# Kernel tuning notes

Hardware: AMD Instinct MI355X
Metric: run time of the kernel (lower is better)

The kernel has to match this reference:

```python
import jax, jax.numpy as jnp
from jax import lax
import numpy as np

B, T, F_IN, H = 64, 128, 12, 128  # batch, seq_len, input/output features, hidden


def _uinit(key, shape, fan):
    return jax.random.uniform(key, shape, jnp.float32, -1.0, 1.0) / np.float32(np.sqrt(fan))


def setup_inputs() -> dict:
    key = jax.random.key(0)
    ks = jax.random.split(key, 12)
    inp = {
        "x": jax.random.normal(ks[0], (B, T, F_IN), jnp.float32),
        # encoder LSTM (gate order i,f,g,o; b = b_ih + b_hh folded together)
        "enc_Wih": _uinit(ks[1], (4 * H, F_IN), H),
        "enc_Whh": _uinit(ks[2], (4 * H, H), H),
        "enc_b": _uinit(ks[3], (4 * H,), H),
        # decoder LSTM (input is the 12-dim teacher-forced x slice)
        "dec_Wih": _uinit(ks[4], (4 * H, F_IN), H),
        "dec_Whh": _uinit(ks[5], (4 * H, H), H),
        "dec_b": _uinit(ks[6], (4 * H,), H),
        # attention: Linear(2H -> H) with bias, then v: Linear(H -> 1, no bias)
        "attn_W": _uinit(ks[7], (H, 2 * H), 2 * H),
        "attn_b": _uinit(ks[8], (H,), 2 * H),
        "v_w": _uinit(ks[9], (H,), H),
        # output layer: Linear(2H -> F_IN)  (intended width; see notes)
        "out_W": _uinit(ks[10], (F_IN, 2 * H), 2 * H),
        "out_b": _uinit(ks[11], (F_IN,), 2 * H),
    }
    return inp


def _lstm_cell(xt, h, c, Wih, Whh, b):
    z = xt @ Wih.T + h @ Whh.T + b  # [B, 4H]
    i, f, g, o = jnp.split(z, 4, axis=-1)
    c = jax.nn.sigmoid(f) * c + jax.nn.sigmoid(i) * jnp.tanh(g)
    h = jax.nn.sigmoid(o) * jnp.tanh(c)
    return h, c


def reference(x, enc_Wih, enc_Whh, enc_b, dec_Wih, dec_Whh, dec_b,
              attn_W, attn_b, v_w, out_W, out_b):
    b_, t_, _ = x.shape
    hdim = enc_Whh.shape[1]
    xs = jnp.swapaxes(x, 0, 1)  # [T, B, F]
    h0 = jnp.zeros((b_, hdim), x.dtype)
    c0 = jnp.zeros((b_, hdim), x.dtype)

    def enc_step(carry, xt):
        h, c = carry
        h, c = _lstm_cell(xt, h, c, enc_Wih, enc_Whh, enc_b)
        return (h, c), h

    (hT, cT), enc_hs = lax.scan(enc_step, (h0, c0), xs)
    enc_out = jnp.swapaxes(enc_hs, 0, 1)  # [B, T, H]

    # split attn weight: cat(hidden, enc_out) @ W.T == hidden@W1.T + enc_out@W2.T
    W1, W2 = attn_W[:, :hdim], attn_W[:, hdim:]
    enc_proj = jnp.einsum("bth,gh->btg", enc_out, W2)  # precompute encoder side

    def dec_step(carry, xt):
        h, c = carry
        h, c = _lstm_cell(xt, h, c, dec_Wih, dec_Whh, dec_b)
        energy = jnp.tanh((h @ W1.T)[:, None, :] + enc_proj + attn_b)  # [B,T,H]
        score = jnp.einsum("bth,h->bt", energy, v_w)
        w = jax.nn.softmax(score, axis=1)  # attention over encoder time
        ctx = jnp.einsum("bt,bth->bh", w, enc_out)
        return (h, c), jnp.concatenate([h, ctx], axis=-1)  # [B, 2H]

    _, dec_ys = lax.scan(dec_step, (hT, cT), xs)
    dec_out = jnp.swapaxes(dec_ys, 0, 1)  # [B, T, 2H]
    return dec_out @ out_W.T + out_b  # [B, T, F]
```

## Files before the change

### kernel.cpp

```cpp
#include <hip/hip_runtime.h>
#include <hip/hip_bf16.h>

#define BB 64
#define TT 128
#define FIN 12
#define HH 128
#define GG 512

#define LOG2E 1.4426950408889634f
#define TWO_LOG2E 2.8853900817779268f

__device__ __forceinline__ float fexp2(float x) { return __builtin_amdgcn_exp2f(x); }
__device__ __forceinline__ float frcp(float x)  { return __builtin_amdgcn_rcpf(x); }

__device__ __forceinline__ float tanh_f(float x) {
  return 1.0f - 2.0f * frcp(1.0f + fexp2(TWO_LOG2E * x));
}
__device__ __forceinline__ float sigm_f(float x) {
  return frcp(1.0f + fexp2(-LOG2E * x));
}

#define FMA4S(acc, s, v) do { \
  acc.x = fmaf((s), (v).x, acc.x); \
  acc.y = fmaf((s), (v).y, acc.y); \
  acc.z = fmaf((s), (v).z, acc.z); \
  acc.w = fmaf((s), (v).w, acc.w); } while (0)

__global__ __launch_bounds__(512, 2) void lstm_kernel(
    const float* __restrict__ x,
    const float* __restrict__ eWih, const float* __restrict__ eWhh, const float* __restrict__ eb,
    const float* __restrict__ dWih, const float* __restrict__ dWhh, const float* __restrict__ db,
    float* __restrict__ encH, float* __restrict__ decH)
{
  const int b = blockIdx.x;
  const int g = threadIdx.x;

  __shared__ __align__(16) float xs[TT * FIN];
  __shared__ __align__(16) float h_lds[HH];
  __shared__ __align__(16) float zact[GG];

  if (g < (TT * FIN / 4))
    ((float4*)xs)[g] = ((const float4*)(x + (size_t)b * TT * FIN))[g];
  if (g < HH) h_lds[g] = 0.0f;
  float c = 0.0f;

  const int gate = g >> 7;

  #pragma unroll 1
  for (int phase = 0; phase < 2; ++phase) {
    const float* Wih  = phase ? dWih : eWih;
    const float* Whh  = phase ? dWhh : eWhh;
    const float* bias = phase ? db : eb;
    float* Hout       = phase ? decH : encH;

    float wih[FIN];
    #pragma unroll
    for (int j = 0; j < 3; ++j) {
      float4 v = *(const float4*)(Wih + g * FIN + 4 * j);
      wih[4*j+0] = v.x; wih[4*j+1] = v.y; wih[4*j+2] = v.z; wih[4*j+3] = v.w;
    }
    float whh[HH];
    #pragma unroll
    for (int j = 0; j < 32; ++j) {
      float4 v = *(const float4*)(Whh + g * HH + 4 * j);
      whh[4*j+0] = v.x; whh[4*j+1] = v.y; whh[4*j+2] = v.z; whh[4*j+3] = v.w;
    }
    const float bz = bias[g];

    #pragma unroll 1
    for (int t = 0; t < TT; ++t) {
      __syncthreads();
      float a0 = bz, a1 = 0.0f, a2 = 0.0f, a3 = 0.0f;
      {
        const float4* xt4 = (const float4*)(xs + t * FIN);
        float4 xa = xt4[0], xb = xt4[1], xc = xt4[2];
        a0 = fmaf(xa.x, wih[0], a0); a1 = fmaf(xa.y, wih[1], a1);
        a2 = fmaf(xa.z, wih[2], a2); a3 = fmaf(xa.w, wih[3], a3);
        a0 = fmaf(xb.x, wih[4], a0); a1 = fmaf(xb.y, wih[5], a1);
        a2 = fmaf(xb.z, wih[6], a2); a3 = fmaf(xb.w, wih[7], a3);
        a0 = fmaf(xc.x, wih[8], a0); a1 = fmaf(xc.y, wih[9], a1);
        a2 = fmaf(xc.z, wih[10], a2); a3 = fmaf(xc.w, wih[11], a3);
      }
      #pragma unroll
      for (int k = 0; k < HH; k += 4) {
        float4 h4 = *(const float4*)&h_lds[k];
        a0 = fmaf(h4.x, whh[k + 0], a0);
        a1 = fmaf(h4.y, whh[k + 1], a1);
        a2 = fmaf(h4.z, whh[k + 2], a2);
        a3 = fmaf(h4.w, whh[k + 3], a3);
      }
      float acc = (a0 + a1) + (a2 + a3);
      zact[g] = (gate == 2) ? tanh_f(acc) : sigm_f(acc);
      __syncthreads();
      if (g < HH) {
        float iv = zact[g], fv = zact[HH + g], gv = zact[2 * HH + g], ov = zact[3 * HH + g];
        c = fmaf(fv, c, iv * gv);
        float hn = ov * tanh_f(c);
        h_lds[g] = hn;
        Hout[((size_t)b * TT + t) * HH + g] = hn;
      }
    }
  }
}

__global__ __launch_bounds__(256, 2) void proj_kernel(
    const float* __restrict__ encH, const float* __restrict__ decH,
    const float* __restrict__ attnW, const float* __restrict__ attnb,
    float* __restrict__ Abuf, float* __restrict__ Pbuf)
{
  const int m  = blockIdx.x & 1;
  const int b  = (blockIdx.x >> 1) & 63;
  const int r0 = (blockIdx.x >> 7) * 16;
  const int tid = threadIdx.x;

  __shared__ __align__(16) float WT[64 * 128];
  __shared__ __align__(16) float Xt[16 * 128];

  const float* X = (m ? encH : decH) + ((size_t)b * TT + r0) * HH;
  const float* W = attnW + (m ? HH : 0);

  ((float4*)Xt)[tid]       = ((const float4*)X)[tid];
  ((float4*)Xt)[256 + tid] = ((const float4*)X)[256 + tid];

  const int hq = tid & 31, rr = tid >> 5;
  const int h0 = 4 * hq;

  float4 acc0, acc1;
  if (m == 0) { acc0 = *(const float4*)(attnb + h0); acc1 = acc0; }
  else        { acc0 = make_float4(0.f, 0.f, 0.f, 0.f); acc1 = acc0; }

  for (int kb = 0; kb < 2; ++kb) {
    __syncthreads();
    {
      int h = tid >> 1, koff = (tid & 1) * 32;
      #pragma unroll
      for (int j = 0; j < 8; ++j) {
        float4 v = *(const float4*)(W + h * 256 + kb * 64 + koff + 4 * j);
        int kp = koff + 4 * j;
        WT[(kp + 0) * 128 + h] = v.x;
        WT[(kp + 1) * 128 + h] = v.y;
        WT[(kp + 2) * 128 + h] = v.z;
        WT[(kp + 3) * 128 + h] = v.w;
      }
    }
    __syncthreads();
    const float* xr0 = Xt + (2 * rr) * 128 + kb * 64;
    const float* xr1 = xr0 + 128;
    #pragma unroll
    for (int k4 = 0; k4 < 64; k4 += 4) {
      float4 xa = *(const float4*)(xr0 + k4);
      float4 xb = *(const float4*)(xr1 + k4);
      float4 w0 = *(const float4*)&WT[(k4 + 0) * 128 + h0];
      float4 w1 = *(const float4*)&WT[(k4 + 1) * 128 + h0];
      float4 w2 = *(const float4*)&WT[(k4 + 2) * 128 + h0];
      float4 w3 = *(const float4*)&WT[(k4 + 3) * 128 + h0];
      FMA4S(acc0, xa.x, w0); FMA4S(acc0, xa.y, w1);
      FMA4S(acc0, xa.z, w2); FMA4S(acc0, xa.w, w3);
      FMA4S(acc1, xb.x, w0); FMA4S(acc1, xb.y, w1);
      FMA4S(acc1, xb.z, w2); FMA4S(acc1, xb.w, w3);
    }
  }
  float* O = (m ? Pbuf : Abuf) + ((size_t)b * TT + r0) * HH;
  *(float4*)(O + (2 * rr) * 128 + h0)     = acc0;
  *(float4*)(O + (2 * rr + 1) * 128 + h0) = acc1;
}

__global__ __launch_bounds__(512, 2) void attn_kernel(
    const float* __restrict__ encH, const float* __restrict__ decH,
    const float* __restrict__ Abuf, const float* __restrict__ Pbuf,
    const float* __restrict__ vw, const float* __restrict__ outW,
    const float* __restrict__ outb, float* __restrict__ out)
{
  const int b  = blockIdx.x >> 3;
  const int s0 = (blockIdx.x & 7) * 16;
  const int tid = threadIdx.x;

  __shared__ __align__(16) float buf[64 * 128];
  __shared__ __align__(16) float a_lds[16 * 128];
  __shared__ __align__(16) float sc[16 * 128];
  __shared__ __align__(16) float dh[16 * 128];
  __shared__ __align__(16) float vl[HH];

  ((float4*)a_lds)[tid] = ((const float4*)(Abuf + ((size_t)b * TT + s0) * HH))[tid];
  ((float4*)dh)[tid]    = ((const float4*)(decH + ((size_t)b * TT + s0) * HH))[tid];
  if (tid < 32) ((float4*)vl)[tid] = ((const float4*)vw)[tid];

  const int u  = tid & 31;
  const int sl = tid >> 5;
  const int uq = u & 15;
  const int uh = u >> 4;

  for (int half = 0; half < 2; ++half) {
    const int tbase = half * 64;
    __syncthreads();
    #pragma unroll
    for (int i = 0; i < 4; ++i) {
      int flat = i * 2048 + tid * 4;
      int tp = flat >> 7;
      int h0 = flat & 127;
      float4 v = *(const float4*)(Pbuf + ((size_t)b * TT + tbase + tp) * HH + h0);
      int tq = tp >> 2, tr = tp & 3;
      buf[(h0 + 0) * 64 + 4 * ((tq ^ ((h0 + 0) >> 2)) & 15) + tr] = v.x;
      buf[(h0 + 1) * 64 + 4 * ((tq ^ ((h0 + 1) >> 2)) & 15) + tr] = v.y;
      buf[(h0 + 2) * 64 + 4 * ((tq ^ ((h0 + 2) >> 2)) & 15) + tr] = v.z;
      buf[(h0 + 3) * 64 + 4 * ((tq ^ ((h0 + 3) >> 2)) & 15) + tr] = v.w;
    }
    __syncthreads();
    float4 acc = make_float4(0.f, 0.f, 0.f, 0.f);
    const float* arow = a_lds + sl * 128;
    #pragma unroll 8
    for (int hh = 0; hh < 64; ++hh) {
      int h = uh * 64 + hh;
      float ah = arow[h];
      float vh = vl[h];
      float4 p4 = *(const float4*)&buf[h * 64 + 4 * ((uq ^ ((h >> 2) & 15)) & 15)];
      acc.x = fmaf(vh, tanh_f(ah + p4.x), acc.x);
      acc.y = fmaf(vh, tanh_f(ah + p4.y), acc.y);
      acc.z = fmaf(vh, tanh_f(ah + p4.z), acc.z);
      acc.w = fmaf(vh, tanh_f(ah + p4.w), acc.w);
    }
    acc.x += __shfl_xor(acc.x, 16, 64);
    acc.y += __shfl_xor(acc.y, 16, 64);
    acc.z += __shfl_xor(acc.z, 16, 64);
    acc.w += __shfl_xor(acc.w, 16, 64);
    if (uh == 0) *(float4*)&sc[sl * 128 + tbase + 4 * uq] = acc;
  }
  __syncthreads();

  {
    float4 sv = *(const float4*)&sc[sl * 128 + 4 * u];
    float mx = fmaxf(fmaxf(sv.x, sv.y), fmaxf(sv.z, sv.w));
    #pragma unroll
    for (int msk = 1; msk <= 16; msk <<= 1) mx = fmaxf(mx, __shfl_xor(mx, msk, 64));
    float4 e;
    e.x = fexp2(LOG2E * (sv.x - mx));
    e.y = fexp2(LOG2E * (sv.y - mx));
    e.z = fexp2(LOG2E * (sv.z - mx));
    e.w = fexp2(LOG2E * (sv.w - mx));
    float sm = (e.x + e.y) + (e.z + e.w);
    #pragma unroll
    for (int msk = 1; msk <= 16; msk <<= 1) sm += __shfl_xor(sm, msk, 64);
    float r = frcp(sm);
    e.x *= r; e.y *= r; e.z *= r; e.w *= r;
    *(float4*)&sc[sl * 128 + 4 * u] = e;
  }

  float4 ctx = make_float4(0.f, 0.f, 0.f, 0.f);
  const int h0c = 4 * u;
  for (int half = 0; half < 2; ++half) {
    const int tbase = half * 64;
    __syncthreads();
    #pragma unroll
    for (int i = 0; i < 4; ++i) {
      int flat = i * 2048 + tid * 4;
      int tp = flat >> 7;
      int hh0 = flat & 127;
      *(float4*)&buf[tp * 128 + hh0] =
          *(const float4*)(encH + ((size_t)b * TT + tbase + tp) * HH + hh0);
    }
    __syncthreads();
    const float* wrow = sc + sl * 128 + tbase;
    #pragma unroll 8
    for (int tp = 0; tp < 64; ++tp) {
      float wt = wrow[tp];
      float4 e4 = *(const float4*)&buf[tp * 128 + h0c];
      FMA4S(ctx, wt, e4);
    }
  }
  __syncthreads();
  *(float4*)&a_lds[sl * 128 + h0c] = ctx;
  __syncthreads();

  if (tid < 192) {
    int s = tid / 12, f = tid % 12;
    float acc = outb[f];
    const float4* w4 = (const float4*)(outW + f * 256);
    const float4* d4 = (const float4*)(dh + s * 128);
    const float4* c4 = (const float4*)(a_lds + s * 128);
    #pragma unroll
    for (int k = 0; k < 32; ++k) {
      float4 wv = w4[k], dv = d4[k];
      acc = fmaf(wv.x, dv.x, acc); acc = fmaf(wv.y, dv.y, acc);
      acc = fmaf(wv.z, dv.z, acc); acc = fmaf(wv.w, dv.w, acc);
    }
    #pragma unroll
    for (int k = 0; k < 32; ++k) {
      float4 wv = w4[32 + k], cv = c4[k];
      acc = fmaf(wv.x, cv.x, acc); acc = fmaf(wv.y, cv.y, acc);
      acc = fmaf(wv.z, cv.z, acc); acc = fmaf(wv.w, cv.w, acc);
    }
    out[((size_t)b * TT + s0 + s) * FIN + f] = acc;
  }
}

extern "C" void kernel_launch(void* const* d_in, const int* in_sizes, int n_in,
                              void* d_out, int out_size, void* d_ws, size_t ws_size,
                              hipStream_t stream)
{
  const float* x     = (const float*)d_in[0];
  const float* eWih  = (const float*)d_in[1];
  const float* eWhh  = (const float*)d_in[2];
  const float* eb    = (const float*)d_in[3];
  const float* dWih  = (const float*)d_in[4];
  const float* dWhh  = (const float*)d_in[5];
  const float* db    = (const float*)d_in[6];
  const float* attnW = (const float*)d_in[7];
  const float* attnb = (const float*)d_in[8];
  const float* vw    = (const float*)d_in[9];
  const float* outW  = (const float*)d_in[10];
  const float* outb  = (const float*)d_in[11];
  float* out = (float*)d_out;

  float* ws   = (float*)d_ws;
  const size_t SEG = (size_t)BB * TT * HH;
  float* encH = ws;
  float* decH = ws + SEG;
  float* Abuf = ws + 2 * SEG;
  float* Pbuf = ws + 3 * SEG;

  lstm_kernel<<<64, 512, 0, stream>>>(x, eWih, eWhh, eb, dWih, dWhh, db, encH, decH);
  proj_kernel<<<1024, 256, 0, stream>>>(encH, decH, attnW, attnb, Abuf, Pbuf);
  attn_kernel<<<512, 512, 0, stream>>>(encH, decH, Abuf, Pbuf, vw, outW, outb, out);
}
```

Baseline: 364.6 us.

## Split LSTM gate dot products across two thread halves with LDS reduction

The LSTM recurrence kernel now launches 1024 threads per batch row instead of 512, and each gate row's 128-wide hidden dot product (plus the 12-wide input part) is split into two halves handled by separate threads. Partial sums go to shared memory, and the 128 cell threads combine them, add bias and apply the activations. This halves the serial FMA chain and the per-thread weight registers on the latency-bound sequential path. In exchange it adds an LDS partial-sum exchange, moves all gate activations onto 128 threads, and runs larger blocks that need more barrier participants.

```diff
diff --git a/kernel.cpp b/kernel.cpp
--- a/kernel.cpp
+++ b/kernel.cpp
@@ -26,25 +26,25 @@
   acc.z = fmaf((s), (v).z, acc.z); \
   acc.w = fmaf((s), (v).w, acc.w); } while (0)
 
-__global__ __launch_bounds__(512, 2) void lstm_kernel(
+__global__ __launch_bounds__(1024, 4) void lstm_kernel(
     const float* __restrict__ x,
     const float* __restrict__ eWih, const float* __restrict__ eWhh, const float* __restrict__ eb,
     const float* __restrict__ dWih, const float* __restrict__ dWhh, const float* __restrict__ db,
     float* __restrict__ encH, float* __restrict__ decH)
 {
-  const int b = blockIdx.x;
-  const int g = threadIdx.x;
+  const int b   = blockIdx.x;
+  const int tid = threadIdx.x;
+  const int g   = tid & 511;
+  const int kh  = tid >> 9;
 
   __shared__ __align__(16) float xs[TT * FIN];
   __shared__ __align__(16) float h_lds[HH];
-  __shared__ __align__(16) float zact[GG];
-
-  if (g < (TT * FIN / 4))
-    ((float4*)xs)[g] = ((const float4*)(x + (size_t)b * TT * FIN))[g];
-  if (g < HH) h_lds[g] = 0.0f;
+  __shared__ __align__(16) float part[2 * GG];
+
+  if (tid < (TT * FIN / 4))
+    ((float4*)xs)[tid] = ((const float4*)(x + (size_t)b * TT * FIN))[tid];
+  if (tid < HH) h_lds[tid] = 0.0f;
   float c = 0.0f;
-
-  const int gate = g >> 7;
 
   #pragma unroll 1
   for (int phase = 0; phase < 2; ++phase) {
@@ -53,51 +53,58 @@
     const float* bias = phase ? db : eb;
     float* Hout       = phase ? decH : encH;
 
-    float wih[FIN];
-    #pragma unroll
-    for (int j = 0; j < 3; ++j) {
-      float4 v = *(const float4*)(Wih + g * FIN + 4 * j);
-      wih[4*j+0] = v.x; wih[4*j+1] = v.y; wih[4*j+2] = v.z; wih[4*j+3] = v.w;
-    }
-    float whh[HH];
-    #pragma unroll
-    for (int j = 0; j < 32; ++j) {
-      float4 v = *(const float4*)(Whh + g * HH + 4 * j);
-      whh[4*j+0] = v.x; whh[4*j+1] = v.y; whh[4*j+2] = v.z; whh[4*j+3] = v.w;
-    }
-    const float bz = bias[g];
+    float4 whh[16];
+    #pragma unroll
+    for (int j = 0; j < 16; ++j)
+      whh[j] = *(const float4*)(Whh + g * HH + kh * 64 + 4 * j);
+    float wih[6];
+    #pragma unroll
+    for (int j = 0; j < 6; ++j)
+      wih[j] = Wih[g * FIN + kh * 6 + j];
+
+    float b_i = 0.f, b_f = 0.f, b_g = 0.f, b_o = 0.f;
+    if (tid < HH) {
+      b_i = bias[tid];
+      b_f = bias[HH + tid];
+      b_g = bias[2 * HH + tid];
+      b_o = bias[3 * HH + tid];
+    }
 
     #pragma unroll 1
     for (int t = 0; t < TT; ++t) {
       __syncthreads();
-      float a0 = bz, a1 = 0.0f, a2 = 0.0f, a3 = 0.0f;
+      float a0, a1, a2 = 0.0f, a3 = 0.0f;
       {
-        const float4* xt4 = (const float4*)(xs + t * FIN);
-        float4 xa = xt4[0], xb = xt4[1], xc = xt4[2];
-        a0 = fmaf(xa.x, wih[0], a0); a1 = fmaf(xa.y, wih[1], a1);
-        a2 = fmaf(xa.z, wih[2], a2); a3 = fmaf(xa.w, wih[3], a3);
-        a0 = fmaf(xb.x, wih[4], a0); a1 = fmaf(xb.y, wih[5], a1);
-        a2 = fmaf(xb.z, wih[6], a2); a3 = fmaf(xb.w, wih[7], a3);
-        a0 = fmaf(xc.x, wih[8], a0); a1 = fmaf(xc.y, wih[9], a1);
-        a2 = fmaf(xc.z, wih[10], a2); a3 = fmaf(xc.w, wih[11], a3);
+        const float2* xt2 = (const float2*)(xs + t * FIN + kh * 6);
+        float2 x0 = xt2[0], x1 = xt2[1], x2 = xt2[2];
+        a0 = x0.x * wih[0]; a1 = x0.y * wih[1];
+        a0 = fmaf(x1.x, wih[2], a0); a1 = fmaf(x1.y, wih[3], a1);
+        a0 = fmaf(x2.x, wih[4], a0); a1 = fmaf(x2.y, wih[5], a1);
       }
+      const float* hbase = h_lds + kh * 64;
       #pragma unroll
-      for (int k = 0; k < HH; k += 4) {
-        float4 h4 = *(const float4*)&h_lds[k];
-        a0 = fmaf(h4.x, whh[k + 0], a0);
-        a1 = fmaf(h4.y, whh[k + 1], a1);
-        a2 = fmaf(h4.z, whh[k + 2], a2);
-        a3 = fmaf(h4.w, whh[k + 3], a3);
+      for (int k = 0; k < 64; k += 4) {
+        float4 h4 = *(const float4*)(hbase + k);
+        a0 = fmaf(h4.x, whh[k >> 2].x, a0);
+        a1 = fmaf(h4.y, whh[k >> 2].y, a1);
+        a2 = fmaf(h4.z, whh[k >> 2].z, a2);
+        a3 = fmaf(h4.w, whh[k >> 2].w, a3);
       }
-      float acc = (a0 + a1) + (a2 + a3);
-      zact[g] = (gate == 2) ? tanh_f(acc) : sigm_f(acc);
+      part[2 * g + kh] = (a0 + a1) + (a2 + a3);
       __syncthreads();
-      if (g < HH) {
-        float iv = zact[g], fv = zact[HH + g], gv = zact[2 * HH + g], ov = zact[3 * HH + g];
-        c = fmaf(fv, c, iv * gv);
-        float hn = ov * tanh_f(c);
-        h_lds[g] = hn;
-        Hout[((size_t)b * TT + t) * HH + g] = hn;
+      if (tid < HH) {
+        float2 pi = *(const float2*)&part[2 * tid];
+        float2 pf = *(const float2*)&part[2 * (HH + tid)];
+        float2 pg = *(const float2*)&part[2 * (2 * HH + tid)];
+        float2 po = *(const float2*)&part[2 * (3 * HH + tid)];
+        float zi = sigm_f(pi.x + pi.y + b_i);
+        float zf = sigm_f(pf.x + pf.y + b_f);
+        float zg = tanh_f(pg.x + pg.y + b_g);
+        float zo = sigm_f(po.x + po.y + b_o);
+        c = fmaf(zf, c, zi * zg);
+        float hn = zo * tanh_f(c);
+        h_lds[tid] = hn;
+        Hout[((size_t)b * TT + t) * HH + tid] = hn;
       }
     }
   }
@@ -318,7 +325,7 @@
   float* Abuf = ws + 2 * SEG;
   float* Pbuf = ws + 3 * SEG;
 
-  lstm_kernel<<<64, 512, 0, stream>>>(x, eWih, eWhh, eb, dWih, dWhh, db, encH, decH);
+  lstm_kernel<<<64, 1024, 0, stream>>>(x, eWih, eWhh, eb, dWih, dWhh, db, encH, decH);
   proj_kernel<<<1024, 256, 0, stream>>>(encH, decH, attnW, attnb, Abuf, Pbuf);
   attn_kernel<<<512, 512, 0, stream>>>(encH, decH, Abuf, Pbuf, vw, outW, outb, out);
 }
```

New measurement: 391.0 us. 1.07x slower.

## Pair LSTM gates per lane with shuffle exchange, one barrier per step

Applied to the files above, without the earlier changes.

The LSTM recurrence kernel now uses 256 threads, with each lane computing two gate rows: lane pairs hold (i,g) and (f,o) for the same hidden unit and swap partial products with a wave shuffle. This removes the zact LDS round trip and the second __syncthreads per timestep, and double-buffers h so a single barrier per step is enough. In exchange each thread keeps 256 weight floats in registers, which raises register pressure and risks spills.

```diff
diff --git a/kernel.cpp b/kernel.cpp
--- a/kernel.cpp
+++ b/kernel.cpp
@@ -26,26 +26,35 @@
   acc.z = fmaf((s), (v).z, acc.z); \
   acc.w = fmaf((s), (v).w, acc.w); } while (0)
 
-__global__ __launch_bounds__(512, 2) void lstm_kernel(
+__global__ __launch_bounds__(256, 1) void lstm_kernel(
     const float* __restrict__ x,
     const float* __restrict__ eWih, const float* __restrict__ eWhh, const float* __restrict__ eb,
     const float* __restrict__ dWih, const float* __restrict__ dWhh, const float* __restrict__ db,
     float* __restrict__ encH, float* __restrict__ decH)
 {
-  const int b = blockIdx.x;
-  const int g = threadIdx.x;
+  const int b    = blockIdx.x;
+  const int tid  = threadIdx.x;
+  const int lane = tid & 63;
+  const int wv   = tid >> 6;
+  const int p    = lane & 1;
+  const int j    = wv * 32 + (lane >> 1);
 
   __shared__ __align__(16) float xs[TT * FIN];
-  __shared__ __align__(16) float h_lds[HH];
-  __shared__ __align__(16) float zact[GG];
-
-  if (g < (TT * FIN / 4))
-    ((float4*)xs)[g] = ((const float4*)(x + (size_t)b * TT * FIN))[g];
-  if (g < HH) h_lds[g] = 0.0f;
+  __shared__ __align__(16) float hbuf[2][HH];
+
+  {
+    const float4* src = (const float4*)(x + (size_t)b * TT * FIN);
+    ((float4*)xs)[tid] = src[tid];
+    if (tid < 128) ((float4*)xs)[256 + tid] = src[256 + tid];
+  }
+  if (tid < HH) { hbuf[0][tid] = 0.0f; hbuf[1][tid] = 0.0f; }
   float c = 0.0f;
 
-  const int gate = g >> 7;
-
+  const int row_a = p * HH + j;
+  const int row_b = (2 + p) * HH + j;
+  const float kact = p ? -LOG2E : TWO_LOG2E;
+
+  int ts = 0;
   #pragma unroll 1
   for (int phase = 0; phase < 2; ++phase) {
     const float* Wih  = phase ? dWih : eWih;
@@ -53,51 +62,80 @@
     const float* bias = phase ? db : eb;
     float* Hout       = phase ? decH : encH;
 
-    float wih[FIN];
-    #pragma unroll
-    for (int j = 0; j < 3; ++j) {
-      float4 v = *(const float4*)(Wih + g * FIN + 4 * j);
-      wih[4*j+0] = v.x; wih[4*j+1] = v.y; wih[4*j+2] = v.z; wih[4*j+3] = v.w;
-    }
-    float whh[HH];
-    #pragma unroll
-    for (int j = 0; j < 32; ++j) {
-      float4 v = *(const float4*)(Whh + g * HH + 4 * j);
-      whh[4*j+0] = v.x; whh[4*j+1] = v.y; whh[4*j+2] = v.z; whh[4*j+3] = v.w;
-    }
-    const float bz = bias[g];
+    float4 wa[32], wb[32];
+    #pragma unroll
+    for (int k = 0; k < 32; ++k) {
+      wa[k] = *(const float4*)(Whh + (size_t)row_a * HH + 4 * k);
+      wb[k] = *(const float4*)(Whh + (size_t)row_b * HH + 4 * k);
+    }
+    float4 xwa[3], xwb[3];
+    #pragma unroll
+    for (int k = 0; k < 3; ++k) {
+      xwa[k] = *(const float4*)(Wih + (size_t)row_a * FIN + 4 * k);
+      xwb[k] = *(const float4*)(Wih + (size_t)row_b * FIN + 4 * k);
+    }
+    const float bza = bias[row_a];
+    const float bzb = bias[row_b];
 
     #pragma unroll 1
-    for (int t = 0; t < TT; ++t) {
+    for (int t = 0; t < TT; ++t, ++ts) {
       __syncthreads();
-      float a0 = bz, a1 = 0.0f, a2 = 0.0f, a3 = 0.0f;
+      const float* hb = hbuf[ts & 1];
+
+      float a0 = bza, a1 = 0.f, a2 = 0.f, a3 = 0.f;
+      float b0 = bzb, b1 = 0.f, b2 = 0.f, b3 = 0.f;
+      #pragma unroll
+      for (int k = 0; k < 32; k += 4) {
+        float4 h0 = *(const float4*)&hb[4 * k];
+        float4 h1 = *(const float4*)&hb[4 * k + 4];
+        float4 h2 = *(const float4*)&hb[4 * k + 8];
+        float4 h3 = *(const float4*)&hb[4 * k + 12];
+        a0 = fmaf(h0.x, wa[k].x, a0);   a1 = fmaf(h0.y, wa[k].y, a1);
+        a2 = fmaf(h0.z, wa[k].z, a2);   a3 = fmaf(h0.w, wa[k].w, a3);
+        b0 = fmaf(h0.x, wb[k].x, b0);   b1 = fmaf(h0.y, wb[k].y, b1);
+        b2 = fmaf(h0.z, wb[k].z, b2);   b3 = fmaf(h0.w, wb[k].w, b3);
+        a0 = fmaf(h1.x, wa[k+1].x, a0); a1 = fmaf(h1.y, wa[k+1].y, a1);
+        a2 = fmaf(h1.z, wa[k+1].z, a2); a3 = fmaf(h1.w, wa[k+1].w, a3);
+        b0 = fmaf(h1.x, wb[k+1].x, b0); b1 = fmaf(h1.y, wb[k+1].y, b1);
+        b2 = fmaf(h1.z, wb[k+1].z, b2); b3 = fmaf(h1.w, wb[k+1].w, b3);
+        a0 = fmaf(h2.x, wa[k+2].x, a0); a1 = fmaf(h2.y, wa[k+2].y, a1);
+        a2 = fmaf(h2.z, wa[k+2].z, a2); a3 = fmaf(h2.w, wa[k+2].w, a3);
+        b0 = fmaf(h2.x, wb[k+2].x, b0); b1 = fmaf(h2.y, wb[k+2].y, b1);
+        b2 = fmaf(h2.z, wb[k+2].z, b2); b3 = fmaf(h2.w, wb[k+2].w, b3);
+        a0 = fmaf(h3.x, wa[k+3].x, a0); a1 = fmaf(h3.y, wa[k+3].y, a1);
+        a2 = fmaf(h3.z, wa[k+3].z, a2); a3 = fmaf(h3.w, wa[k+3].w, a3);
+        b0 = fmaf(h3.x, wb[k+3].x, b0); b1 = fmaf(h3.y, wb[k+3].y, b1);
+        b2 = fmaf(h3.z, wb[k+3].z, b2); b3 = fmaf(h3.w, wb[k+3].w, b3);
+      }
       {
-        const float4* xt4 = (const float4*)(xs + t * FIN);
-        float4 xa = xt4[0], xb = xt4[1], xc = xt4[2];
-        a0 = fmaf(xa.x, wih[0], a0); a1 = fmaf(xa.y, wih[1], a1);
-        a2 = fmaf(xa.z, wih[2], a2); a3 = fmaf(xa.w, wih[3], a3);
-        a0 = fmaf(xb.x, wih[4], a0); a1 = fmaf(xb.y, wih[5], a1);
-        a2 = fmaf(xb.z, wih[6], a2); a3 = fmaf(xb.w, wih[7], a3);
-        a0 = fmaf(xc.x, wih[8], a0); a1 = fmaf(xc.y, wih[9], a1);
-        a2 = fmaf(xc.z, wih[10], a2); a3 = fmaf(xc.w, wih[11], a3);
+        const float4* xt = (const float4*)(xs + t * FIN);
+        float4 x0 = xt[0], x1 = xt[1], x2 = xt[2];
+        a0 = fmaf(x0.x, xwa[0].x, a0); a1 = fmaf(x0.y, xwa[0].y, a1);
+        a2 = fmaf(x0.z, xwa[0].z, a2); a3 = fmaf(x0.w, xwa[0].w, a3);
+        a0 = fmaf(x1.x, xwa[1].x, a0); a1 = fmaf(x1.y, xwa[1].y, a1);
+        a2 = fmaf(x1.z, xwa[1].z, a2); a3 = fmaf(x1.w, xwa[1].w, a3);
+        a0 = fmaf(x2.x, xwa[2].x, a0); a1 = fmaf(x2.y, xwa[2].y, a1);
+        a2 = fmaf(x2.z, xwa[2].z, a2); a3 = fmaf(x2.w, xwa[2].w, a3);
+        b0 = fmaf(x0.x, xwb[0].x, b0); b1 = fmaf(x0.y, xwb[0].y, b1);
+        b2 = fmaf(x0.z, xwb[0].z, b2); b3 = fmaf(x0.w, xwb[0].w, b3);
+        b0 = fmaf(x1.x, xwb[1].x, b0); b1 = fmaf(x1.y, xwb[1].y, b1);
+        b2 = fmaf(x1.z, xwb[1].z, b2); b3 = fmaf(x1.w, xwb[1].w, b3);
+        b0 = fmaf(x2.x, xwb[2].x, b0); b1 = fmaf(x2.y, xwb[2].y, b1);
+        b2 = fmaf(x2.z, xwb[2].z, b2); b3 = fmaf(x2.w, xwb[2].w, b3);
       }
-      #pragma unroll
-      for (int k = 0; k < HH; k += 4) {
-        float4 h4 = *(const float4*)&h_lds[k];
-        a0 = fmaf(h4.x, whh[k + 0], a0);
-        a1 = fmaf(h4.y, whh[k + 1], a1);
-        a2 = fmaf(h4.z, whh[k + 2], a2);
-        a3 = fmaf(h4.w, whh[k + 3], a3);
-      }
-      float acc = (a0 + a1) + (a2 + a3);
-      zact[g] = (gate == 2) ? tanh_f(acc) : sigm_f(acc);
-      __syncthreads();
-      if (g < HH) {
-        float iv = zact[g], fv = zact[HH + g], gv = zact[2 * HH + g], ov = zact[3 * HH + g];
-        c = fmaf(fv, c, iv * gv);
-        float hn = ov * tanh_f(c);
-        h_lds[g] = hn;
-        Hout[((size_t)b * TT + t) * HH + g] = hn;
+      float za = (a0 + a1) + (a2 + a3);
+      float zb = (b0 + b1) + (b2 + b3);
+
+      float sa = sigm_f(za);
+      float r  = frcp(1.0f + fexp2(kact * zb));
+      float vb = p ? r : 1.0f - 2.0f * r;
+      float u  = sa * vb;
+      float ux = __shfl_xor(u, 1, 64);
+      if (p) {
+        c = fmaf(sa, c, ux);
+        float hn = vb * tanh_f(c);
+        hbuf[(ts + 1) & 1][j] = hn;
+        Hout[((size_t)b * TT + t) * HH + j] = hn;
       }
     }
   }
@@ -318,7 +356,7 @@
   float* Abuf = ws + 2 * SEG;
   float* Pbuf = ws + 3 * SEG;
 
-  lstm_kernel<<<64, 512, 0, stream>>>(x, eWih, eWhh, eb, dWih, dWhh, db, encH, decH);
+  lstm_kernel<<<64, 256, 0, stream>>>(x, eWih, eWhh, eb, dWih, dWhh, db, encH, decH);
   proj_kernel<<<1024, 256, 0, stream>>>(encH, decH, attnW, attnb, Abuf, Pbuf);
   attn_kernel<<<512, 512, 0, stream>>>(encH, decH, Abuf, Pbuf, vw, outW, outb, out);
 }
```

After: 634.1 us. 73.9% more time.

## Batch LSTM recurrence across 16 sequences per block using split-bf16 MFMA

Applied to the files above, without the earlier changes.

The LSTM recurrence now processes 16 batch rows per block and computes the gate matmul with bf16 MFMA instructions. Precision is kept near fp32 by splitting weights and h into hi/lo bf16 pairs and summing three products. The input projection and bias are folded into an extra MFMA K-tile, h is double-buffered in LDS so each step needs only one barrier, and global h stores are deferred by one step. The grid shrinks from 64 blocks to 4, so per-step latency matters more than throughput, and the split-bf16 scheme adds some approximation error.

```diff
diff --git a/kernel.cpp b/kernel.cpp
--- a/kernel.cpp
+++ b/kernel.cpp
@@ -5,11 +5,17 @@
 #define TT 128
 #define FIN 12
 #define HH 128
-#define GG 512
+#define BT 16
+#define SROW 136
 
 #define LOG2E 1.4426950408889634f
 #define TWO_LOG2E 2.8853900817779268f
 
+typedef __attribute__((ext_vector_type(8))) short bf16x8;
+typedef __attribute__((ext_vector_type(4))) float f32x4;
+
+#define MFMA(a, b, c) __builtin_amdgcn_mfma_f32_16x16x32_bf16((a), (b), (c), 0, 0, 0)
+
 __device__ __forceinline__ float fexp2(float x) { return __builtin_amdgcn_exp2f(x); }
 __device__ __forceinline__ float frcp(float x)  { return __builtin_amdgcn_rcpf(x); }
 
@@ -18,6 +24,18 @@
 }
 __device__ __forceinline__ float sigm_f(float x) {
   return frcp(1.0f + fexp2(-LOG2E * x));
+}
+
+__device__ __forceinline__ unsigned short bfhi(float v) {
+  unsigned u = __float_as_uint(v);
+  return (unsigned short)((u + 0x7FFFu + ((u >> 16) & 1u)) >> 16);
+}
+__device__ __forceinline__ float bf2f(unsigned short h) {
+  return __uint_as_float((unsigned)h << 16);
+}
+__device__ __forceinline__ void bfsplit(float v, unsigned short& hi, unsigned short& lo) {
+  hi = bfhi(v);
+  lo = bfhi(v - bf2f(hi));
 }
 
 #define FMA4S(acc, s, v) do { \
@@ -32,75 +50,177 @@
     const float* __restrict__ dWih, const float* __restrict__ dWhh, const float* __restrict__ db,
     float* __restrict__ encH, float* __restrict__ decH)
 {
-  const int b = blockIdx.x;
-  const int g = threadIdx.x;
-
-  __shared__ __align__(16) float xs[TT * FIN];
-  __shared__ __align__(16) float h_lds[HH];
-  __shared__ __align__(16) float zact[GG];
-
-  if (g < (TT * FIN / 4))
-    ((float4*)xs)[g] = ((const float4*)(x + (size_t)b * TT * FIN))[g];
-  if (g < HH) h_lds[g] = 0.0f;
-  float c = 0.0f;
-
-  const int gate = g >> 7;
+  const int bb0  = blockIdx.x * BT;
+  const int tid  = threadIdx.x;
+  const int w    = tid >> 6;
+  const int lane = tid & 63;
+  const int bcol = lane & 15;
+  const int quad = lane >> 4;
+
+  __shared__ __align__(16) unsigned short sbuf[2][2][BT][SROW];
+
+  {
+    unsigned* p = (unsigned*)sbuf;
+    for (int idx = tid; idx < (2 * 2 * BT * SROW / 2); idx += 512) p[idx] = 0;
+  }
+
+  float xc[8];
+  {
+    const float* xb = x + (size_t)(bb0 + bcol) * TT * FIN;
+    if (quad == 0) {
+      float4 a = *(const float4*)xb, b2 = *(const float4*)(xb + 4);
+      xc[0]=a.x; xc[1]=a.y; xc[2]=a.z; xc[3]=a.w; xc[4]=b2.x; xc[5]=b2.y; xc[6]=b2.z; xc[7]=b2.w;
+    } else if (quad == 1) {
+      float4 a = *(const float4*)(xb + 8);
+      xc[0]=a.x; xc[1]=a.y; xc[2]=a.z; xc[3]=a.w; xc[4]=0; xc[5]=0; xc[6]=0; xc[7]=0;
+    } else {
+      #pragma unroll
+      for (int j = 0; j < 8; ++j) xc[j] = 0.0f;
+    }
+  }
+  __syncthreads();
+
+  const int arow = w * 16 + (lane & 15);
+
+  float c0 = 0.f, c1 = 0.f, c2 = 0.f, c3 = 0.f;
+  float hp0 = 0.f, hp1 = 0.f, hp2 = 0.f, hp3 = 0.f;
 
   #pragma unroll 1
   for (int phase = 0; phase < 2; ++phase) {
     const float* Wih  = phase ? dWih : eWih;
     const float* Whh  = phase ? dWhh : eWhh;
     const float* bias = phase ? db : eb;
-    float* Hout       = phase ? decH : encH;
-
-    float wih[FIN];
-    #pragma unroll
-    for (int j = 0; j < 3; ++j) {
-      float4 v = *(const float4*)(Wih + g * FIN + 4 * j);
-      wih[4*j+0] = v.x; wih[4*j+1] = v.y; wih[4*j+2] = v.z; wih[4*j+3] = v.w;
-    }
-    float whh[HH];
-    #pragma unroll
-    for (int j = 0; j < 32; ++j) {
-      float4 v = *(const float4*)(Whh + g * HH + 4 * j);
-      whh[4*j+0] = v.x; whh[4*j+1] = v.y; whh[4*j+2] = v.z; whh[4*j+3] = v.w;
-    }
-    const float bz = bias[g];
+
+    bf16x8 Ahi[4][5], Alo[4][5];
+    #pragma unroll
+    for (int g = 0; g < 4; ++g) {
+      const float* wr = Whh + (size_t)(g * HH + arow) * HH + quad * 8;
+      #pragma unroll
+      for (int kt = 0; kt < 4; ++kt) {
+        float4 v0 = *(const float4*)(wr + kt * 32);
+        float4 v1 = *(const float4*)(wr + kt * 32 + 4);
+        float vv[8] = {v0.x, v0.y, v0.z, v0.w, v1.x, v1.y, v1.z, v1.w};
+        bf16x8 h8, l8;
+        #pragma unroll
+        for (int j = 0; j < 8; ++j) {
+          unsigned short hi, lo; bfsplit(vv[j], hi, lo);
+          h8[j] = (short)hi; l8[j] = (short)lo;
+        }
+        Ahi[g][kt] = h8; Alo[g][kt] = l8;
+      }
+      {
+        float vv[8] = {0, 0, 0, 0, 0, 0, 0, 0};
+        if (quad == 0) {
+          const float* wir = Wih + (size_t)(g * HH + arow) * FIN;
+          #pragma unroll
+          for (int j = 0; j < 8; ++j) vv[j] = wir[j];
+        } else if (quad == 1) {
+          const float* wir = Wih + (size_t)(g * HH + arow) * FIN + 8;
+          #pragma unroll
+          for (int j = 0; j < 4; ++j) vv[j] = wir[j];
+          vv[4] = bias[g * HH + arow];
+        }
+        bf16x8 h8, l8;
+        #pragma unroll
+        for (int j = 0; j < 8; ++j) {
+          unsigned short hi, lo; bfsplit(vv[j], hi, lo);
+          h8[j] = (short)hi; l8[j] = (short)lo;
+        }
+        Ahi[g][4] = h8; Alo[g][4] = l8;
+      }
+    }
 
     #pragma unroll 1
     for (int t = 0; t < TT; ++t) {
+      const int ts  = phase * TT + t;
+      const int cur = ts & 1, nxt = cur ^ 1;
       __syncthreads();
-      float a0 = bz, a1 = 0.0f, a2 = 0.0f, a3 = 0.0f;
+
+      if (ts > 0) {
+        const int tsp = ts - 1;
+        float* Hp = (tsp >> 7) ? decH : encH;
+        *(float4*)(Hp + ((size_t)(bb0 + bcol) * TT + (tsp & 127)) * HH + w * 16 + quad * 4)
+            = make_float4(hp0, hp1, hp2, hp3);
+      }
+
+      float xn[8] = {0, 0, 0, 0, 0, 0, 0, 0};
       {
-        const float4* xt4 = (const float4*)(xs + t * FIN);
-        float4 xa = xt4[0], xb = xt4[1], xc = xt4[2];
-        a0 = fmaf(xa.x, wih[0], a0); a1 = fmaf(xa.y, wih[1], a1);
-        a2 = fmaf(xa.z, wih[2], a2); a3 = fmaf(xa.w, wih[3], a3);
-        a0 = fmaf(xb.x, wih[4], a0); a1 = fmaf(xb.y, wih[5], a1);
-        a2 = fmaf(xb.z, wih[6], a2); a3 = fmaf(xb.w, wih[7], a3);
-        a0 = fmaf(xc.x, wih[8], a0); a1 = fmaf(xc.y, wih[9], a1);
-        a2 = fmaf(xc.z, wih[10], a2); a3 = fmaf(xc.w, wih[11], a3);
-      }
+        const int tn = (ts + 1) & 127;
+        const float* xb = x + (size_t)(bb0 + bcol) * TT * FIN + tn * FIN;
+        if (quad == 0) {
+          float4 a = *(const float4*)xb, b2 = *(const float4*)(xb + 4);
+          xn[0]=a.x; xn[1]=a.y; xn[2]=a.z; xn[3]=a.w; xn[4]=b2.x; xn[5]=b2.y; xn[6]=b2.z; xn[7]=b2.w;
+        } else if (quad == 1) {
+          float4 a = *(const float4*)(xb + 8);
+          xn[0]=a.x; xn[1]=a.y; xn[2]=a.z; xn[3]=a.w;
+        }
+      }
+
+      bf16x8 bxh = {0,0,0,0,0,0,0,0}, bxl = {0,0,0,0,0,0,0,0};
+      if (quad == 0) {
+        #pragma unroll
+        for (int j = 0; j < 8; ++j) {
+          unsigned short hi, lo; bfsplit(xc[j], hi, lo);
+          bxh[j] = (short)hi; bxl[j] = (short)lo;
+        }
+      } else if (quad == 1) {
+        #pragma unroll
+        for (int j = 0; j < 4; ++j) {
+          unsigned short hi, lo; bfsplit(xc[j], hi, lo);
+          bxh[j] = (short)hi; bxl[j] = (short)lo;
+        }
+        bxh[4] = (short)0x3F80;
+      }
+
+      f32x4 acc0 = {0,0,0,0}, acc1 = {0,0,0,0}, acc2 = {0,0,0,0}, acc3 = {0,0,0,0};
+      const unsigned short* sb_hi = &sbuf[cur][0][bcol][quad * 8];
+      const unsigned short* sb_lo = &sbuf[cur][1][bcol][quad * 8];
       #pragma unroll
-      for (int k = 0; k < HH; k += 4) {
-        float4 h4 = *(const float4*)&h_lds[k];
-        a0 = fmaf(h4.x, whh[k + 0], a0);
-        a1 = fmaf(h4.y, whh[k + 1], a1);
-        a2 = fmaf(h4.z, whh[k + 2], a2);
-        a3 = fmaf(h4.w, whh[k + 3], a3);
-      }
-      float acc = (a0 + a1) + (a2 + a3);
-      zact[g] = (gate == 2) ? tanh_f(acc) : sigm_f(acc);
-      __syncthreads();
-      if (g < HH) {
-        float iv = zact[g], fv = zact[HH + g], gv = zact[2 * HH + g], ov = zact[3 * HH + g];
-        c = fmaf(fv, c, iv * gv);
-        float hn = ov * tanh_f(c);
-        h_lds[g] = hn;
-        Hout[((size_t)b * TT + t) * HH + g] = hn;
-      }
-    }
-  }
+      for (int kt = 0; kt < 4; ++kt) {
+        bf16x8 bh = *(const bf16x8*)(sb_hi + kt * 32);
+        bf16x8 bl = *(const bf16x8*)(sb_lo + kt * 32);
+        acc0 = MFMA(Ahi[0][kt], bh, acc0); acc1 = MFMA(Ahi[1][kt], bh, acc1);
+        acc2 = MFMA(Ahi[2][kt], bh, acc2); acc3 = MFMA(Ahi[3][kt], bh, acc3);
+        acc0 = MFMA(Alo[0][kt], bh, acc0); acc1 = MFMA(Alo[1][kt], bh, acc1);
+        acc2 = MFMA(Alo[2][kt], bh, acc2); acc3 = MFMA(Alo[3][kt], bh, acc3);
+        acc0 = MFMA(Ahi[0][kt], bl, acc0); acc1 = MFMA(Ahi[1][kt], bl, acc1);
+        acc2 = MFMA(Ahi[2][kt], bl, acc2); acc3 = MFMA(Ahi[3][kt], bl, acc3);
+      }
+      acc0 = MFMA(Ahi[0][4], bxh, acc0); acc1 = MFMA(Ahi[1][4], bxh, acc1);
+      acc2 = MFMA(Ahi[2][4], bxh, acc2); acc3 = MFMA(Ahi[3][4], bxh, acc3);
+      acc0 = MFMA(Alo[0][4], bxh, acc0); acc1 = MFMA(Alo[1][4], bxh, acc1);
+      acc2 = MFMA(Alo[2][4], bxh, acc2); acc3 = MFMA(Alo[3][4], bxh, acc3);
+      acc0 = MFMA(Ahi[0][4], bxl, acc0); acc1 = MFMA(Ahi[1][4], bxl, acc1);
+      acc2 = MFMA(Ahi[2][4], bxl, acc2); acc3 = MFMA(Ahi[3][4], bxl, acc3);
+
+      unsigned short hh[4], hl[4];
+      {
+        float zi, zf, zg, zo;
+        zi = sigm_f(acc0[0]); zf = sigm_f(acc1[0]); zg = tanh_f(acc2[0]); zo = sigm_f(acc3[0]);
+        c0 = fmaf(zf, c0, zi * zg); hp0 = zo * tanh_f(c0); bfsplit(hp0, hh[0], hl[0]);
+        zi = sigm_f(acc0[1]); zf = sigm_f(acc1[1]); zg = tanh_f(acc2[1]); zo = sigm_f(acc3[1]);
+        c1 = fmaf(zf, c1, zi * zg); hp1 = zo * tanh_f(c1); bfsplit(hp1, hh[1], hl[1]);
+        zi = sigm_f(acc0[2]); zf = sigm_f(acc1[2]); zg = tanh_f(acc2[2]); zo = sigm_f(acc3[2]);
+        c2 = fmaf(zf, c2, zi * zg); hp2 = zo * tanh_f(c2); bfsplit(hp2, hh[2], hl[2]);
+        zi = sigm_f(acc0[3]); zf = sigm_f(acc1[3]); zg = tanh_f(acc2[3]); zo = sigm_f(acc3[3]);
+        c3 = fmaf(zf, c3, zi * zg); hp3 = zo * tanh_f(c3); bfsplit(hp3, hh[3], hl[3]);
+      }
+
+      {
+        unsigned long long ph = (unsigned long long)hh[0] | ((unsigned long long)hh[1] << 16)
+                              | ((unsigned long long)hh[2] << 32) | ((unsigned long long)hh[3] << 48);
+        unsigned long long pl = (unsigned long long)hl[0] | ((unsigned long long)hl[1] << 16)
+                              | ((unsigned long long)hl[2] << 32) | ((unsigned long long)hl[3] << 48);
+        *(unsigned long long*)&sbuf[nxt][0][bcol][w * 16 + quad * 4] = ph;
+        *(unsigned long long*)&sbuf[nxt][1][bcol][w * 16 + quad * 4] = pl;
+      }
+
+      #pragma unroll
+      for (int j = 0; j < 8; ++j) xc[j] = xn[j];
+    }
+  }
+  *(float4*)(decH + ((size_t)(bb0 + bcol) * TT + 127) * HH + w * 16 + quad * 4)
+      = make_float4(hp0, hp1, hp2, hp3);
 }
 
 __global__ __launch_bounds__(256, 2) void proj_kernel(
@@ -318,7 +438,7 @@
   float* Abuf = ws + 2 * SEG;
   float* Pbuf = ws + 3 * SEG;
 
-  lstm_kernel<<<64, 512, 0, stream>>>(x, eWih, eWhh, eb, dWih, dWhh, db, encH, decH);
+  lstm_kernel<<<4, 512, 0, stream>>>(x, eWih, eWhh, eb, dWih, dWhh, db, encH, decH);
   proj_kernel<<<1024, 256, 0, stream>>>(encH, decH, attnW, attnb, Abuf, Pbuf);
   attn_kernel<<<512, 512, 0, stream>>>(encH, decH, Abuf, Pbuf, vw, outW, outb, out);
 }
```

Result: slower. 702.1 us (+92.5%).
